# Performance work log

Hardware: AMD Instinct MI355X
Metric: run time of the kernel (lower is better)

Reference implementation:

```python
import jax, jax.numpy as jnp
import numpy as np

H = 256          # hidden_size
L = 2            # num_layers
K = 4            # khops
R = 128          # relation_num
N_NODES = 20000
N_EDGES = 160000
N_LG_EDGES = 640000


def setup_inputs() -> dict:
    key = jax.random.key(0)
    ks = iter(jax.random.split(key, 40))
    def nrm(shape, s=1.0):
        return jax.random.normal(next(ks), shape, dtype=jnp.float32) * s
    w = 1.0 / float(np.sqrt(H))
    return {
        "x": nrm((N_NODES, H)),
        "edge_feat": jax.random.randint(next(ks), (N_EDGES,), 0, R),
        "edge_index_g": jax.random.randint(next(ks), (2, N_EDGES), 0, N_NODES),
        "edge_index_lg": jax.random.randint(next(ks), (2, N_LG_EDGES), 0, N_EDGES),
        "rel_embed": nrm((R, H)),
        # per-layer, per-core (0=node update, 1=edge update) parameter stacks
        "w_self": nrm((L, 2, H, H), w), "b_self": jnp.zeros((L, 2, H), jnp.float32),
        "w_khop": nrm((L, 2, K, H, H), w), "b_khop": jnp.zeros((L, 2, K, H), jnp.float32),
        "w_fuse": nrm((L, 2, H, H), w), "b_fuse": jnp.zeros((L, 2, H), jnp.float32),
        "w_ff1": nrm((L, 2, H, 4 * H), w), "b_ff1": jnp.zeros((L, 2, 4 * H), jnp.float32),
        "w_ff2": nrm((L, 2, 4 * H, H), 1.0 / float(np.sqrt(4 * H))), "b_ff2": jnp.zeros((L, 2, H), jnp.float32),
        "ln1_g": jnp.ones((L, 2, H), jnp.float32), "ln1_b": jnp.zeros((L, 2, H), jnp.float32),
        "ln2_g": jnp.ones((L, 2, H), jnp.float32), "ln2_b": jnp.zeros((L, 2, H), jnp.float32),
    }


def _layernorm(x, g, b, eps=1e-5):
    m = jnp.mean(x, axis=-1, keepdims=True)
    v = jnp.var(x, axis=-1, keepdims=True)
    return (x - m) * jax.lax.rsqrt(v + eps) * g + b


def _core(p, src, dst, x, fused):
    """LGNNCore.forward (eval mode, dropout never applied in core)."""
    (ws, bs, wk, bk, wf, bf, w1, b1, w2, b2, g1, c1, g2, c2) = p
    n = x.shape[0]
    prev = x @ ws + bs
    # k-hop copy_src + sum aggregation, each hop gets its own linear
    z = x
    kh = jnp.zeros_like(prev)
    for i in range(wk.shape[0]):
        z = jax.ops.segment_sum(z[src], dst, num_segments=n)
        kh = kh + z @ wk[i] + bk[i]
    edge = fused @ wf + bf
    out = jax.nn.gelu(prev + kh + edge, approximate=False)
    out = _layernorm(x + out, g1, c1)
    ffn = jax.nn.gelu(out @ w1 + b1, approximate=False) @ w2 + b2
    return _layernorm(out + ffn, g2, c2)


def reference(x, edge_feat, edge_index_g, edge_index_lg, rel_embed,
              w_self, b_self, w_khop, b_khop, w_fuse, b_fuse,
              w_ff1, b_ff1, w_ff2, b_ff2, ln1_g, ln1_b, ln2_g, ln2_b):
    lg_x = rel_embed[edge_feat]                       # [n_edges, H]
    src_g, dst_g = edge_index_g[0], edge_index_g[1]
    src_l, dst_l = edge_index_lg[0], edge_index_lg[1]
    n_nodes = x.shape[0]
    for l in range(w_self.shape[0]):
        def pick(c):
            return (w_self[l, c], b_self[l, c], w_khop[l, c], b_khop[l, c],
                    w_fuse[l, c], b_fuse[l, c], w_ff1[l, c], b_ff1[l, c],
                    w_ff2[l, c], b_ff2[l, c], ln1_g[l, c], ln1_b[l, c],
                    ln2_g[l, c], ln2_b[l, c])
        # pmpd @ lg_x : scatter each edge feature to both of its endpoints
        fused_nodes = (jax.ops.segment_sum(lg_x, src_g, num_segments=n_nodes)
                       + jax.ops.segment_sum(lg_x, dst_g, num_segments=n_nodes))
        # pmpd^T @ x : gather both endpoint node features per edge
        fused_edges = x[src_g] + x[dst_g]
        new_x = _core(pick(0), src_g, dst_g, x, fused_nodes)
        new_lg_x = _core(pick(1), src_l, dst_l, lg_x, fused_edges)
        x, lg_x = new_x, new_lg_x
    return x, lg_x
```

## Files before the change

### kernel.cpp

```cpp
#include <hip/hip_runtime.h>

typedef __bf16 bf16;
typedef __attribute__((ext_vector_type(8))) __bf16 bf16x8;
typedef __attribute__((ext_vector_type(4))) __bf16 bf16x4;
typedef __attribute__((ext_vector_type(4))) float f32x4;

#define HD 256
#define GEMM_GELU 2

__device__ __forceinline__ float gelu_f(float x) {
  float x2 = x * x;
  float u = 1.5957691216057308f * x * fmaf(0.044715f, x2, 1.0f);
  float e = __expf(-u);
  return x / (1.0f + e);
}

__device__ __forceinline__ void gload_lds16(const void* g, void* l) {
  __builtin_amdgcn_global_load_lds(
      (const __attribute__((address_space(1))) unsigned int*)g,
      (__attribute__((address_space(3))) unsigned int*)l, 16, 0, 0);
}

__global__ __launch_bounds__(256) void gemm_k(
    const bf16* __restrict__ A, const bf16* __restrict__ Wt,
    const float* __restrict__ bias, bf16* __restrict__ C,
    int M, int Kd, int lda, int ldc, int flags)
{
  __shared__ __align__(16) bf16 sA[3][128 * 32];
  __shared__ __align__(16) bf16 sB[3][128 * 32];
  const int t = threadIdx.x;
  const int lane = t & 63, w = t >> 6;
  const int n0 = blockIdx.x * 128, m0 = blockIdx.y * 128;
  const int wr = w >> 1, wc = w & 1;
  const int lm = lane & 15, quad = lane >> 4;

  const int srow = t >> 2;
  const int cg = (t & 3) ^ ((t >> 3) & 3);
  const bool full = (m0 + 128 <= M);

  const char* a0 = (const char*)(A + (size_t)(m0 + srow) * lda) + cg * 16;
  const char* a1 = (const char*)(A + (size_t)(m0 + srow + 64) * lda) + cg * 16;
  const char* b0 = (const char*)(Wt + (size_t)(n0 + srow) * Kd) + cg * 16;
  const char* b1 = (const char*)(Wt + (size_t)(n0 + srow) * Kd) + (size_t)64 * Kd * 2 + cg * 16;

  const int soff = (quad ^ ((lm >> 1) & 3)) * 8;

  f32x4 acc[4][4];
#pragma unroll
  for (int i = 0; i < 4; i++)
#pragma unroll
    for (int j = 0; j < 4; j++)
#pragma unroll
      for (int r = 0; r < 4; r++) acc[i][j][r] = 0.f;

  const int nk = Kd >> 5;

  auto stage = [&](bf16* SA, bf16* SB, int kt) {
    size_t ko = (size_t)kt * 64;
    gload_lds16(a0 + ko, SA + w * 512);
    gload_lds16(a1 + ko, SA + 2048 + w * 512);
    gload_lds16(b0 + ko, SB + w * 512);
    gload_lds16(b1 + ko, SB + 2048 + w * 512);
  };

  auto compute = [&](const bf16* SA, const bf16* SB) {
    bf16x8 af[4], bv[4];
#pragma unroll
    for (int i = 0; i < 4; i++) af[i] = *(const bf16x8*)(SA + (wr * 64 + i * 16 + lm) * 32 + soff);
#pragma unroll
    for (int j = 0; j < 4; j++) bv[j] = *(const bf16x8*)(SB + (wc * 64 + j * 16 + lm) * 32 + soff);
#pragma unroll
    for (int i = 0; i < 4; i++)
#pragma unroll
      for (int j = 0; j < 4; j++)
        acc[i][j] = __builtin_amdgcn_mfma_f32_16x16x32_bf16(bv[j], af[i], acc[i][j], 0, 0, 0);
  };

  if (full) {
    stage(sA[0], sB[0], 0);
    if (nk > 1) stage(sA[1], sB[1], 1);
    for (int kt = 0; kt < nk; ++kt) {
      int cb = kt % 3;
      int nxt = kt + 2;
      if (nxt < nk) {
        stage(sA[nxt % 3], sB[nxt % 3], nxt);
        asm volatile("s_waitcnt vmcnt(8)" ::: "memory");
      } else if (nxt == nk) {
        asm volatile("s_waitcnt vmcnt(4)" ::: "memory");
      } else {
        asm volatile("s_waitcnt vmcnt(0)" ::: "memory");
      }
      __builtin_amdgcn_s_barrier();
      asm volatile("" ::: "memory");
      compute(sA[cb], sB[cb]);
      __builtin_amdgcn_s_barrier();
      asm volatile("" ::: "memory");
    }
  } else {
    for (int kt = 0; kt < nk; ++kt) {
      size_t ko = (size_t)kt * 64;
#pragma unroll
      for (int c = 0; c < 2; c++) {
        int row = srow + c * 64;
        int gr = m0 + row;
        bf16x8 va;
#pragma unroll
        for (int q = 0; q < 8; q++) va[q] = (bf16)0.f;
        if (gr < M) va = *(const bf16x8*)((const char*)(A + (size_t)gr * lda) + ko + cg * 16);
        *(bf16x8*)(sA[0] + row * 32 + (t & 3) * 8) = va;
      }
      gload_lds16(b0 + ko, sB[0] + w * 512);
      gload_lds16(b1 + ko, sB[0] + 2048 + w * 512);
      __syncthreads();
      compute(sA[0], sB[0]);
      __syncthreads();
    }
  }

  float4 bia[4];
#pragma unroll
  for (int j = 0; j < 4; j++)
    bia[j] = *(const float4*)(bias + n0 + wc * 64 + j * 16 + quad * 4);
#pragma unroll
  for (int i = 0; i < 4; i++) {
    int gr = m0 + wr * 64 + i * 16 + lm;
    if (gr < M) {
      bf16* crow = C + (size_t)gr * ldc;
#pragma unroll
      for (int j = 0; j < 4; j++) {
        int gc = n0 + wc * 64 + j * 16 + quad * 4;
        float v0 = acc[i][j][0] + bia[j].x;
        float v1 = acc[i][j][1] + bia[j].y;
        float v2 = acc[i][j][2] + bia[j].z;
        float v3 = acc[i][j][3] + bia[j].w;
        if (flags & GEMM_GELU) {
          v0 = gelu_f(v0); v1 = gelu_f(v1); v2 = gelu_f(v2); v3 = gelu_f(v3);
        }
        bf16x4 o = {(bf16)v0, (bf16)v1, (bf16)v2, (bf16)v3};
        *(bf16x4*)(crow + gc) = o;
      }
    }
  }
}

__global__ __launch_bounds__(256) void segsum_k(
    const int* __restrict__ offs, const int* __restrict__ cols,
    const bf16* __restrict__ in, int ldin, bf16* __restrict__ out, int ldout, int nseg)
{
  int wid = threadIdx.x >> 6, lane = threadIdx.x & 63;
  int seg = blockIdx.x * 4 + wid;
  if (seg >= nseg) return;
  int b = offs[seg], e = offs[seg + 1];
  float a0 = 0.f, a1 = 0.f, a2 = 0.f, a3 = 0.f;
  for (int i = b; i < e; i++) {
    int c = cols[i];
    bf16x4 v = *(const bf16x4*)(in + (size_t)c * ldin + lane * 4);
    a0 += (float)v.x; a1 += (float)v.y; a2 += (float)v.z; a3 += (float)v.w;
  }
  bf16x4 o = {(bf16)a0, (bf16)a1, (bf16)a2, (bf16)a3};
  *(bf16x4*)(out + (size_t)seg * ldout + lane * 4) = o;
}

__global__ __launch_bounds__(256) void ln_k(
    const bf16* __restrict__ X, int ldx, const bf16* __restrict__ A,
    const float* __restrict__ gam, const float* __restrict__ bet,
    bf16* __restrict__ outb, float* __restrict__ outf, int M, int apply_gelu)
{
  int wid = threadIdx.x >> 6, lane = threadIdx.x & 63;
  int row = blockIdx.x * 4 + wid;
  if (row >= M) return;
  size_t xbase = (size_t)row * ldx + lane * 4;
  size_t abase = (size_t)row * HD + lane * 4;
  bf16x4 xv = *(const bf16x4*)(X + xbase);
  bf16x4 av = *(const bf16x4*)(A + abase);
  float s0, s1, s2, s3;
  if (apply_gelu) {
    s0 = (float)xv.x + gelu_f((float)av.x);
    s1 = (float)xv.y + gelu_f((float)av.y);
    s2 = (float)xv.z + gelu_f((float)av.z);
    s3 = (float)xv.w + gelu_f((float)av.w);
  } else {
    s0 = (float)xv.x + (float)av.x;
    s1 = (float)xv.y + (float)av.y;
    s2 = (float)xv.z + (float)av.z;
    s3 = (float)xv.w + (float)av.w;
  }
  float sum = s0 + s1 + s2 + s3;
#pragma unroll
  for (int o = 32; o; o >>= 1) sum += __shfl_xor(sum, o, 64);
  float mean = sum * (1.0f / 256.0f);
  float d0 = s0 - mean, d1 = s1 - mean, d2 = s2 - mean, d3 = s3 - mean;
  float vs = d0 * d0 + d1 * d1 + d2 * d2 + d3 * d3;
#pragma unroll
  for (int o = 32; o; o >>= 1) vs += __shfl_xor(vs, o, 64);
  float rstd = rsqrtf(vs * (1.0f / 256.0f) + 1e-5f);
  float4 g = *(const float4*)(gam + lane * 4);
  float4 bb = *(const float4*)(bet + lane * 4);
  float y0 = d0 * rstd * g.x + bb.x;
  float y1 = d1 * rstd * g.y + bb.y;
  float y2 = d2 * rstd * g.z + bb.z;
  float y3 = d3 * rstd * g.w + bb.w;
  if (outb) {
    bf16x4 o = {(bf16)y0, (bf16)y1, (bf16)y2, (bf16)y3};
    *(bf16x4*)(outb + xbase) = o;
  }
  if (outf) {
    float4 o = {y0, y1, y2, y3};
    *(float4*)(outf + abase) = o;
  }
}

__global__ __launch_bounds__(256) void gather_rel_k(
    const int* __restrict__ feat, const float* __restrict__ rel,
    bf16* __restrict__ out, int ldout, int NE)
{
  int wid = threadIdx.x >> 6, lane = threadIdx.x & 63;
  int e = blockIdx.x * 4 + wid;
  if (e >= NE) return;
  int f = feat[e];
  float4 v = *(const float4*)(rel + (size_t)f * HD + lane * 4);
  bf16x4 o = {(bf16)v.x, (bf16)v.y, (bf16)v.z, (bf16)v.w};
  *(bf16x4*)(out + (size_t)e * ldout + lane * 4) = o;
}

__global__ __launch_bounds__(256) void gather2_k(
    const int* __restrict__ src, const int* __restrict__ dst,
    const bf16* __restrict__ x, int ldx, bf16* __restrict__ out, int ldout, int NE)
{
  int wid = threadIdx.x >> 6, lane = threadIdx.x & 63;
  int e = blockIdx.x * 4 + wid;
  if (e >= NE) return;
  int s = src[e], d = dst[e];
  bf16x4 a = *(const bf16x4*)(x + (size_t)s * ldx + lane * 4);
  bf16x4 b = *(const bf16x4*)(x + (size_t)d * ldx + lane * 4);
  bf16x4 o = {(bf16)((float)a.x + (float)b.x), (bf16)((float)a.y + (float)b.y),
              (bf16)((float)a.z + (float)b.z), (bf16)((float)a.w + (float)b.w)};
  *(bf16x4*)(out + (size_t)e * ldout + lane * 4) = o;
}

__global__ __launch_bounds__(256) void f2b_k(const float* __restrict__ in,
                                             bf16* __restrict__ out, int ldout, int M) {
  int wid = threadIdx.x >> 6, lane = threadIdx.x & 63;
  int row = blockIdx.x * 4 + wid;
  if (row >= M) return;
  float4 v = *(const float4*)(in + (size_t)row * HD + lane * 4);
  bf16x4 o = {(bf16)v.x, (bf16)v.y, (bf16)v.z, (bf16)v.w};
  *(bf16x4*)(out + (size_t)row * ldout + lane * 4) = o;
}

__global__ __launch_bounds__(256) void wtrans_k(const float* __restrict__ in, bf16* __restrict__ out,
                                                int Kd, int Nd) {
  size_t moff = (size_t)blockIdx.y * Kd * Nd;
  int id = blockIdx.x * 256 + threadIdx.x;
  if (id >= Kd * Nd) return;
  int n = id / Kd, k = id - n * Kd;
  out[moff + id] = (bf16)in[moff + (size_t)k * Nd + n];
}

__global__ __launch_bounds__(256) void wcat_k(const float* __restrict__ ws, const float* __restrict__ wk,
                                              const float* __restrict__ wf, bf16* __restrict__ out,
                                              int KH, int CW) {
  int mi = blockIdx.y;
  int id = blockIdx.x * 256 + threadIdx.x;
  if (id >= HD * CW) return;
  int n = id / CW, k = id - n * CW;
  int s = k >> 8, kk = k & 255;
  float v;
  if (s == 0)       v = ws[((size_t)mi * HD + kk) * HD + n];
  else if (s <= KH) v = wk[(((size_t)mi * KH + (s - 1)) * HD + kk) * HD + n];
  else              v = wf[((size_t)mi * HD + kk) * HD + n];
  out[(size_t)mi * HD * CW + id] = (bf16)v;
}

__global__ __launch_bounds__(256) void bcat_k(const float* __restrict__ bs, const float* __restrict__ bk,
                                              const float* __restrict__ bf, float* __restrict__ out, int KH) {
  int mi = blockIdx.x, n = threadIdx.x;
  float v = bs[(size_t)mi * HD + n] + bf[(size_t)mi * HD + n];
  for (int i = 0; i < KH; i++) v += bk[((size_t)mi * KH + i) * HD + n];
  out[(size_t)mi * HD + n] = v;
}

__global__ __launch_bounds__(256) void count_k(const int* __restrict__ keys, int n, int* __restrict__ cnt) {
  int i = blockIdx.x * 256 + threadIdx.x;
  if (i < n) atomicAdd(&cnt[keys[i]], 1);
}
__global__ __launch_bounds__(256) void scan1_k(const int* __restrict__ in, int* __restrict__ out,
                                               int* __restrict__ bsum, int n) {
  __shared__ int sh[256];
  int t = threadIdx.x;
  int i0 = blockIdx.x * 1024 + t * 4;
  int v0 = (i0 < n) ? in[i0] : 0;
  int v1 = (i0 + 1 < n) ? in[i0 + 1] : 0;
  int v2 = (i0 + 2 < n) ? in[i0 + 2] : 0;
  int v3 = (i0 + 3 < n) ? in[i0 + 3] : 0;
  int tsum = v0 + v1 + v2 + v3;
  sh[t] = tsum;
  __syncthreads();
  for (int o = 1; o < 256; o <<= 1) {
    int x = (t >= o) ? sh[t - o] : 0;
    __syncthreads();
    sh[t] += x;
    __syncthreads();
  }
  int e0 = sh[t] - tsum;
  if (t == 255) bsum[blockIdx.x] = sh[255];
  if (i0 < n) out[i0] = e0;
  e0 += v0;
  if (i0 + 1 < n) out[i0 + 1] = e0;
  e0 += v1;
  if (i0 + 2 < n) out[i0 + 2] = e0;
  e0 += v2;
  if (i0 + 3 < n) out[i0 + 3] = e0;
}
__global__ void scan2_k(int* bsum, int nb, int* total) {
  if (threadIdx.x == 0 && blockIdx.x == 0) {
    int acc = 0;
    for (int i = 0; i < nb; i++) { int v = bsum[i]; bsum[i] = acc; acc += v; }
    *total = acc;
  }
}
__global__ __launch_bounds__(256) void scan3_k(int* out, const int* bsum, int n) {
  int i = blockIdx.x * 256 + threadIdx.x;
  if (i < n) out[i] += bsum[i >> 10];
}
__global__ __launch_bounds__(256) void fill_k(const int* __restrict__ keys, const int* __restrict__ vals,
                                              int n, int modE, int* __restrict__ cursor, int* __restrict__ cols) {
  int i = blockIdx.x * 256 + threadIdx.x;
  if (i >= n) return;
  int pos = atomicAdd(&cursor[keys[i]], 1);
  cols[pos] = vals ? vals[i] : (i < modE ? i : i - modE);
}

extern "C" void kernel_launch(void* const* d_in, const int* in_sizes, int n_in,
                              void* d_out, int out_size, void* d_ws, size_t ws_size,
                              hipStream_t stream)
{
  const float* x_in      = (const float*)d_in[0];
  const int*   edge_feat = (const int*)d_in[1];
  const int*   eig       = (const int*)d_in[2];
  const int*   eil       = (const int*)d_in[3];
  const float* rel       = (const float*)d_in[4];
  const float* w_self = (const float*)d_in[5];
  const float* b_self = (const float*)d_in[6];
  const float* w_khop = (const float*)d_in[7];
  const float* b_khop = (const float*)d_in[8];
  const float* w_fuse = (const float*)d_in[9];
  const float* b_fuse = (const float*)d_in[10];
  const float* w_ff1  = (const float*)d_in[11];
  const float* b_ff1  = (const float*)d_in[12];
  const float* w_ff2  = (const float*)d_in[13];
  const float* b_ff2  = (const float*)d_in[14];
  const float* ln1_g  = (const float*)d_in[15];
  const float* ln1_b  = (const float*)d_in[16];
  const float* ln2_g  = (const float*)d_in[17];
  const float* ln2_b  = (const float*)d_in[18];

  const int NN = in_sizes[0] / HD;
  const int NE = in_sizes[1];
  const int NL = in_sizes[3] / 2;
  const int L  = in_sizes[5] / (2 * HD * HD);
  const int KH = in_sizes[7] / (L * 2 * HD * HD);
  const int CW = (KH + 2) * HD;

  char* p = (char*)d_ws;
  auto alloc = [&](size_t bytes) -> void* {
    void* r = (void*)p;
    p += (bytes + 255) & ~(size_t)255;
    return r;
  };

  bf16* n_cat  = (bf16*)alloc((size_t)NN * CW * 2);
  bf16* lg_cat = (bf16*)alloc((size_t)NE * CW * 2);
  bf16* acc_n  = (bf16*)alloc((size_t)NN * HD * 2);
  bf16* acc_e  = (bf16*)alloc((size_t)NE * HD * 2);

  bf16*  wcat_t = (bf16*)alloc((size_t)L * 2 * HD * CW * 2);
  float* bcat   = (float*)alloc((size_t)L * 2 * HD * 4);
  bf16*  wff1_t = (bf16*)alloc((size_t)L * 2 * HD * 4 * HD * 2);
  bf16*  wff2_t = (bf16*)alloc((size_t)L * 2 * HD * 4 * HD * 2);

  int* inc_offs = (int*)alloc((size_t)(NN + 1) * 4);
  int* inc_cur  = (int*)alloc((size_t)NN * 4);
  int* inc_cols = (int*)alloc((size_t)2 * NE * 4);
  int* ng_offs  = (int*)alloc((size_t)(NN + 1) * 4);
  int* ng_cur   = (int*)alloc((size_t)NN * 4);
  int* ng_cols  = (int*)alloc((size_t)NE * 4);
  int* lg_offs  = (int*)alloc((size_t)(NE + 1) * 4);
  int* lg_cur   = (int*)alloc((size_t)NE * 4);
  int* lg_cols  = (int*)alloc((size_t)NL * 4);
  int* bsum     = (int*)alloc(3 * 256 * 4);

  wcat_k<<<dim3((HD * CW + 255) / 256, L * 2), 256, 0, stream>>>(w_self, w_khop, w_fuse, wcat_t, KH, CW);
  bcat_k<<<L * 2, 256, 0, stream>>>(b_self, b_khop, b_fuse, bcat, KH);
  wtrans_k<<<dim3((HD * 4 * HD + 255) / 256, L * 2), 256, 0, stream>>>(w_ff1, wff1_t, HD, 4 * HD);
  wtrans_k<<<dim3((HD * 4 * HD + 255) / 256, L * 2), 256, 0, stream>>>(w_ff2, wff2_t, 4 * HD, HD);

  f2b_k<<<(NN + 3) / 4, 256, 0, stream>>>(x_in, n_cat, CW, NN);
  gather_rel_k<<<(NE + 3) / 4, 256, 0, stream>>>(edge_feat, rel, lg_cat, CW, NE);

  auto build_csr = [&](const int* keys, int nkeys, const int* vals, int modE,
                       int nseg, int* offs, int* cur, int* cols, int* bs) {
    int nb = (nseg + 1023) / 1024;
    hipMemsetAsync(offs, 0, (size_t)(nseg + 1) * 4, stream);
    count_k<<<(nkeys + 255) / 256, 256, 0, stream>>>(keys, nkeys, offs);
    scan1_k<<<nb, 256, 0, stream>>>(offs, offs, bs, nseg);
    scan2_k<<<1, 1, 0, stream>>>(bs, nb, offs + nseg);
    scan3_k<<<(nseg + 255) / 256, 256, 0, stream>>>(offs, bs, nseg);
    hipMemcpyAsync(cur, offs, (size_t)nseg * 4, hipMemcpyDeviceToDevice, stream);
    fill_k<<<(nkeys + 255) / 256, 256, 0, stream>>>(keys, vals, nkeys, modE, cur, cols);
  };
  build_csr(eig, 2 * NE, nullptr, NE, NN, inc_offs, inc_cur, inc_cols, bsum);
  build_csr(eig + NE, NE, eig, 0, NN, ng_offs, ng_cur, ng_cols, bsum + 256);
  build_csr(eil + NL, NL, eil, 0, NE, lg_offs, lg_cur, lg_cols, bsum + 512);

  float* out_x  = (float*)d_out;
  float* out_lg = (float*)d_out + (size_t)NN * HD;

  auto run_core = [&](bf16* cat, bf16* accb, const int* coffs, const int* ccols,
                      int M, int l, int c, float* outf) {
    size_t mi = (size_t)(l * 2 + c);
    int mb = (M + 127) / 128;
    for (int i = 1; i <= KH; i++)
      segsum_k<<<(M + 3) / 4, 256, 0, stream>>>(coffs, ccols, cat + (size_t)(i - 1) * HD, CW,
                                                cat + (size_t)i * HD, CW, M);
    gemm_k<<<dim3(2, mb), 256, 0, stream>>>(cat, wcat_t + mi * HD * CW, bcat + mi * HD,
                                            accb, M, CW, CW, HD, 0);
    ln_k<<<(M + 3) / 4, 256, 0, stream>>>(cat, CW, accb, ln1_g + mi * HD, ln1_b + mi * HD,
                                          cat, (float*)nullptr, M, 1);
    bf16* hid = cat + HD;
    int FC = (M > 40000) ? 40000 : M;
    for (int c0 = 0; c0 < M; c0 += FC) {
      int mc = (M - c0 < FC) ? (M - c0) : FC;
      int mbc = (mc + 127) / 128;
      gemm_k<<<dim3(8, mbc), 256, 0, stream>>>(cat + (size_t)c0 * CW, wff1_t + mi * HD * 4 * HD,
                                               b_ff1 + mi * 4 * HD, hid, mc, HD, CW, CW, GEMM_GELU);
      gemm_k<<<dim3(2, mbc), 256, 0, stream>>>(hid, wff2_t + mi * 4 * HD * HD, b_ff2 + mi * HD,
                                               accb + (size_t)c0 * HD, mc, 4 * HD, CW, HD, 0);
    }
    ln_k<<<(M + 3) / 4, 256, 0, stream>>>(cat, CW, accb, ln2_g + mi * HD, ln2_b + mi * HD,
                                          cat, outf, M, 0);
  };

  for (int l = 0; l < L; l++) {
    segsum_k<<<(NN + 3) / 4, 256, 0, stream>>>(inc_offs, inc_cols, lg_cat, CW,
                                               n_cat + (size_t)(KH + 1) * HD, CW, NN);
    gather2_k<<<(NE + 3) / 4, 256, 0, stream>>>(eig, eig + NE, n_cat, CW,
                                                lg_cat + (size_t)(KH + 1) * HD, CW, NE);
    run_core(n_cat, acc_n, ng_offs, ng_cols, NN, l, 0, (l == L - 1) ? out_x : nullptr);
    run_core(lg_cat, acc_e, lg_offs, lg_cols, NE, l, 1, (l == L - 1) ? out_lg : nullptr);
  }
}
```

Baseline: 3.316 ms.

## Use 64-wide K tiles with double buffering and XOR swizzle in GEMM

The GEMM kernel's K tile grows from 32 to 64, and the LDS pipeline drops from three stages to two (double buffering). The swizzle changes to an 8-column XOR pattern. Each iteration now issues eight async global-to-LDS loads per thread and two MFMA sub-steps, halving the number of barriers per K. In exchange, prefetch depth is lower, which can leave memory latency exposed, and the LDS footprint per block is larger.

```diff
diff --git a/kernel.cpp b/kernel.cpp
--- a/kernel.cpp
+++ b/kernel.cpp
@@ -26,24 +26,22 @@
     const float* __restrict__ bias, bf16* __restrict__ C,
     int M, int Kd, int lda, int ldc, int flags)
 {
-  __shared__ __align__(16) bf16 sA[3][128 * 32];
-  __shared__ __align__(16) bf16 sB[3][128 * 32];
+  __shared__ __align__(16) bf16 sA[2][128 * 64];
+  __shared__ __align__(16) bf16 sB[2][128 * 64];
   const int t = threadIdx.x;
   const int lane = t & 63, w = t >> 6;
   const int n0 = blockIdx.x * 128, m0 = blockIdx.y * 128;
   const int wr = w >> 1, wc = w & 1;
   const int lm = lane & 15, quad = lane >> 4;
 
-  const int srow = t >> 2;
-  const int cg = (t & 3) ^ ((t >> 3) & 3);
+  const int rowl = lane >> 3;
+  const int gcl = (lane & 7) ^ rowl;
   const bool full = (m0 + 128 <= M);
 
-  const char* a0 = (const char*)(A + (size_t)(m0 + srow) * lda) + cg * 16;
-  const char* a1 = (const char*)(A + (size_t)(m0 + srow + 64) * lda) + cg * 16;
-  const char* b0 = (const char*)(Wt + (size_t)(n0 + srow) * Kd) + cg * 16;
-  const char* b1 = (const char*)(Wt + (size_t)(n0 + srow) * Kd) + (size_t)64 * Kd * 2 + cg * 16;
-
-  const int soff = (quad ^ ((lm >> 1) & 3)) * 8;
+  const char* pa = (const char*)(A + (size_t)(m0 + w * 32 + rowl) * lda) + gcl * 16;
+  const char* pb = (const char*)(Wt + (size_t)(n0 + w * 32 + rowl) * Kd) + gcl * 16;
+  const size_t stepA = (size_t)8 * lda * 2;
+  const size_t stepB = (size_t)8 * Kd * 2;
 
   f32x4 acc[4][4];
 #pragma unroll
@@ -53,64 +51,69 @@
 #pragma unroll
       for (int r = 0; r < 4; r++) acc[i][j][r] = 0.f;
 
-  const int nk = Kd >> 5;
+  const int nk = Kd >> 6;
 
   auto stage = [&](bf16* SA, bf16* SB, int kt) {
-    size_t ko = (size_t)kt * 64;
-    gload_lds16(a0 + ko, SA + w * 512);
-    gload_lds16(a1 + ko, SA + 2048 + w * 512);
-    gload_lds16(b0 + ko, SB + w * 512);
-    gload_lds16(b1 + ko, SB + 2048 + w * 512);
+    size_t ko = (size_t)kt * 128;
+#pragma unroll
+    for (int i = 0; i < 4; i++)
+      gload_lds16(pa + i * stepA + ko, SA + w * 2048 + i * 512);
+#pragma unroll
+    for (int i = 0; i < 4; i++)
+      gload_lds16(pb + i * stepB + ko, SB + w * 2048 + i * 512);
   };
 
   auto compute = [&](const bf16* SA, const bf16* SB) {
-    bf16x8 af[4], bv[4];
-#pragma unroll
-    for (int i = 0; i < 4; i++) af[i] = *(const bf16x8*)(SA + (wr * 64 + i * 16 + lm) * 32 + soff);
-#pragma unroll
-    for (int j = 0; j < 4; j++) bv[j] = *(const bf16x8*)(SB + (wc * 64 + j * 16 + lm) * 32 + soff);
-#pragma unroll
-    for (int i = 0; i < 4; i++)
-#pragma unroll
-      for (int j = 0; j < 4; j++)
-        acc[i][j] = __builtin_amdgcn_mfma_f32_16x16x32_bf16(bv[j], af[i], acc[i][j], 0, 0, 0);
+#pragma unroll
+    for (int s = 0; s < 2; s++) {
+      const int soff = ((s * 4 + quad) ^ (lm & 7)) * 8;
+      bf16x8 af[4], bv[4];
+#pragma unroll
+      for (int i = 0; i < 4; i++) af[i] = *(const bf16x8*)(SA + (wr * 64 + i * 16 + lm) * 64 + soff);
+#pragma unroll
+      for (int j = 0; j < 4; j++) bv[j] = *(const bf16x8*)(SB + (wc * 64 + j * 16 + lm) * 64 + soff);
+#pragma unroll
+      for (int i = 0; i < 4; i++)
+#pragma unroll
+        for (int j = 0; j < 4; j++)
+          acc[i][j] = __builtin_amdgcn_mfma_f32_16x16x32_bf16(bv[j], af[i], acc[i][j], 0, 0, 0);
+    }
   };
 
   if (full) {
     stage(sA[0], sB[0], 0);
-    if (nk > 1) stage(sA[1], sB[1], 1);
     for (int kt = 0; kt < nk; ++kt) {
-      int cb = kt % 3;
-      int nxt = kt + 2;
+      int nxt = kt + 1;
       if (nxt < nk) {
-        stage(sA[nxt % 3], sB[nxt % 3], nxt);
+        stage(sA[nxt & 1], sB[nxt & 1], nxt);
         asm volatile("s_waitcnt vmcnt(8)" ::: "memory");
-      } else if (nxt == nk) {
-        asm volatile("s_waitcnt vmcnt(4)" ::: "memory");
       } else {
         asm volatile("s_waitcnt vmcnt(0)" ::: "memory");
       }
       __builtin_amdgcn_s_barrier();
       asm volatile("" ::: "memory");
-      compute(sA[cb], sB[cb]);
+      compute(sA[kt & 1], sB[kt & 1]);
       __builtin_amdgcn_s_barrier();
       asm volatile("" ::: "memory");
     }
   } else {
     for (int kt = 0; kt < nk; ++kt) {
-      size_t ko = (size_t)kt * 64;
-#pragma unroll
-      for (int c = 0; c < 2; c++) {
-        int row = srow + c * 64;
+      size_t ko = (size_t)kt * 128;
+#pragma unroll
+      for (int c = 0; c < 4; c++) {
+        int sid = t + c * 256;
+        int row = sid >> 3, sc = sid & 7;
+        int gc = sc ^ (row & 7);
         int gr = m0 + row;
         bf16x8 va;
 #pragma unroll
         for (int q = 0; q < 8; q++) va[q] = (bf16)0.f;
-        if (gr < M) va = *(const bf16x8*)((const char*)(A + (size_t)gr * lda) + ko + cg * 16);
-        *(bf16x8*)(sA[0] + row * 32 + (t & 3) * 8) = va;
+        if (gr < M) va = *(const bf16x8*)((const char*)(A + (size_t)gr * lda) + ko + gc * 16);
+        *(bf16x8*)(sA[0] + row * 64 + sc * 8) = va;
       }
-      gload_lds16(b0 + ko, sB[0] + w * 512);
-      gload_lds16(b1 + ko, sB[0] + 2048 + w * 512);
+#pragma unroll
+      for (int i = 0; i < 4; i++)
+        gload_lds16(pb + i * stepB + ko, sB[0] + w * 2048 + i * 512);
       __syncthreads();
       compute(sA[0], sB[0]);
       __syncthreads();
```

New measurement: 3.293 ms. Within noise of the previous version (-0.7%).
